# Kernel optimization log

Measured on AMD Instinct MI355X. Metric: run time of the kernel, lower is better.

## Reference

```python
import jax, jax.numpy as jnp
import numpy as np

N_NODES = 50000
N_EDGES = 800000
HID = 128


def setup_inputs() -> dict:
    key = jax.random.key(0)
    ks = jax.random.split(key, 10)
    s_msg = 1.0 / np.sqrt(2 * HID + 1)
    s_u1 = 1.0 / np.sqrt(2 * HID)
    s_u2 = 1.0 / np.sqrt(HID)
    return {
        "z": jax.random.normal(ks[0], (N_NODES, HID), dtype=jnp.float32),
        "edge_weight": jax.random.uniform(ks[1], (N_EDGES,), dtype=jnp.float32),
        "edge_src": jax.random.randint(ks[2], (N_EDGES,), 0, N_NODES),
        "edge_dst": jax.random.randint(ks[3], (N_EDGES,), 0, N_NODES),
        "Wm": jax.random.normal(ks[4], (2 * HID + 1, HID), dtype=jnp.float32) * s_msg,
        "bm": jax.random.normal(ks[5], (HID,), dtype=jnp.float32) * s_msg,
        "W1": jax.random.normal(ks[6], (2 * HID, HID), dtype=jnp.float32) * s_u1,
        "b1": jax.random.normal(ks[7], (HID,), dtype=jnp.float32) * s_u1,
        "W2": jax.random.normal(ks[8], (HID, HID), dtype=jnp.float32) * s_u2,
        "b2": jax.random.normal(ks[9], (HID,), dtype=jnp.float32) * s_u2,
    }


def reference(z, edge_weight, edge_src, edge_dst, Wm, bm, W1, b1, W2, b2):
    n, H = z.shape
    # message Linear on concat([z[u], z[v], w]) split to avoid materializing [E, 2H+1]
    Wd, Ws, ww = Wm[:H], Wm[H:2 * H], Wm[2 * H]  # [H,H], [H,H], [H]
    msgs = (z[edge_dst] @ Wd + z[edge_src] @ Ws
            + edge_weight[:, None] * ww[None, :] + bm)  # [E, H]
    # max-aggregate messages per destination node; zeros for isolated nodes
    agg = jax.ops.segment_max(msgs, edge_dst, num_segments=n)  # [n, H], -inf if empty
    deg = jax.ops.segment_sum(jnp.ones_like(edge_weight), edge_dst, num_segments=n)
    agg = jnp.where(deg[:, None] > 0, agg, jnp.zeros((), dtype=z.dtype))
    # update MLP on concat([z, agg]) split into two GEMMs
    W1a, W1b = W1[:H], W1[H:]
    hidden = jax.nn.relu(z @ W1a + agg @ W1b + b1)  # [n, H]
    return hidden @ W2 + b2  # [n, H]
```

## Files before the change

### kernel.cpp

```cpp
#include <hip/hip_runtime.h>
#include <hip/hip_bf16.h>

#define HID 128

typedef short bf16x8 __attribute__((ext_vector_type(8)));
typedef float f32x4  __attribute__((ext_vector_type(4)));
typedef unsigned short u16;
typedef unsigned long long u64;

__device__ __forceinline__ u16 f2bf(float f) {
    __hip_bfloat16 h = __float2bfloat16(f);
    return *reinterpret_cast<u16*>(&h);
}
__device__ __forceinline__ float bf2f(u16 x) {
    unsigned u = ((unsigned)x) << 16;
    return __uint_as_float(u);
}
__device__ __forceinline__ u64 pack_rec(int dst, int src, float w) {
    int wq = (int)fmaf(w, 32768.f, 0.5f);
    wq = wq > 32767 ? 32767 : wq;
    return ((u64)(unsigned)dst << 31) | ((unsigned)src << 15) | (unsigned)wq;
}


__global__ __launch_bounds__(256)
void hist_kernel(const int* __restrict__ edst, int* __restrict__ bhist,
                 int E, int nbk)
{
    __shared__ int lh[256];
    const int b = blockIdx.x;
    const int t = threadIdx.x;
    lh[t] = 0;
    __syncthreads();
    const int e0 = b * 4096;
    const int eend = min(e0 + 4096, E);
    for (int e = e0 + t; e < eend; e += 256)
        atomicAdd(&lh[edst[e] >> 8], 1);
    __syncthreads();
    if (t < nbk && lh[t] > 0) atomicAdd(&bhist[t], lh[t]);
}

__global__ __launch_bounds__(256)
void cast_scatter(const float* __restrict__ z, const float* __restrict__ Wm,
                  const float* __restrict__ W1, const float* __restrict__ W2,
                  const int* __restrict__ esrc, const int* __restrict__ edst,
                  const float* __restrict__ ew,
                  const int* __restrict__ bhist, int* __restrict__ brun,
                  u16* __restrict__ Ab, u16* __restrict__ Wt, u64* __restrict__ tmp,
                  int N, int Mp, int E, int bz, int bw, int nbk)
{
    const int b = blockIdx.x;
    const int t = threadIdx.x;
    if (b < bz) {
        const int idx8 = (b * 256 + t) * 8;
        const int row = idx8 >> 7, col = idx8 & 127;
        bf16x8 u;
        if (row < N) {
            const float4 v0 = *(const float4*)&z[(size_t)row * 128 + col];
            const float4 v1 = *(const float4*)&z[(size_t)row * 128 + col + 4];
            u[0] = (short)f2bf(v0.x); u[1] = (short)f2bf(v0.y);
            u[2] = (short)f2bf(v0.z); u[3] = (short)f2bf(v0.w);
            u[4] = (short)f2bf(v1.x); u[5] = (short)f2bf(v1.y);
            u[6] = (short)f2bf(v1.z); u[7] = (short)f2bf(v1.w);
        } else { u = bf16x8{0,0,0,0,0,0,0,0}; }
        *(bf16x8*)&Ab[(size_t)row * 256 + col] = u;
    } else if (b < bz + bw) {
        const int idx = (b - bz) * 256 + t;
        float v;
        if (idx < 32768) {
            const int nn = idx >> 7, k = idx & 127;
            v = (nn < 128) ? Wm[k * 128 + nn] : Wm[(128 + k) * 128 + (nn - 128)];
        } else if (idx < 65536) {
            const int j = idx - 32768, n = j >> 8, k = j & 255;
            v = W1[k * 128 + n];
        } else {
            const int j = idx - 65536, n = j >> 7, k = j & 127;
            v = W2[k * 128 + n];
        }
        Wt[idx] = f2bf(v);
    } else {
        __shared__ int cnt[256];
        __shared__ int rbase[256];
        __shared__ int bbase[256];
        __shared__ int ps[256];
        const int e0 = (b - bz - bw) * 4096;
        const int eend = min(e0 + 4096, E);

        const int h = (t < nbk) ? bhist[t] : 0;
        ps[t] = h;
        __syncthreads();
        for (int off = 1; off < 256; off <<= 1) {
            int add = (t >= off) ? ps[t - off] : 0;
            __syncthreads();
            ps[t] += add;
            __syncthreads();
        }
        bbase[t] = ps[t] - h;
        cnt[t] = 0;
        __syncthreads();

        if (eend - e0 == 4096) {
            int myb[16]; u64 myrec[16];
#pragma unroll
            for (int i = 0; i < 16; i++) {
                const int e = e0 + t + i * 256;
                const int d = edst[e];
                myb[i] = d >> 8;
                myrec[i] = pack_rec(d, esrc[e], ew[e]);
                atomicAdd(&cnt[myb[i]], 1);
            }
            __syncthreads();
            if (t < nbk && cnt[t] > 0) rbase[t] = bbase[t] + atomicAdd(&brun[t], cnt[t]);
            __syncthreads();
            cnt[t] = 0;
            __syncthreads();
#pragma unroll
            for (int i = 0; i < 16; i++) {
                const int r = atomicAdd(&cnt[myb[i]], 1);
                tmp[(size_t)rbase[myb[i]] + r] = myrec[i];
            }
        } else {
            for (int e = e0 + t; e < eend; e += 256)
                atomicAdd(&cnt[edst[e] >> 8], 1);
            __syncthreads();
            if (t < nbk && cnt[t] > 0) rbase[t] = bbase[t] + atomicAdd(&brun[t], cnt[t]);
            __syncthreads();
            cnt[t] = 0;
            __syncthreads();
            for (int e = e0 + t; e < eend; e += 256) {
                const int d = edst[e];
                const int bk = d >> 8;
                const int r = atomicAdd(&cnt[bk], 1);
                tmp[(size_t)rbase[bk] + r] = pack_rec(d, esrc[e], ew[e]);
            }
        }
    }
}

__global__ __launch_bounds__(256)
void sort_gemmP(const u64* __restrict__ tmp, const int* __restrict__ bhist,
                int* __restrict__ offsets, unsigned* __restrict__ s_ew,
                int N, int E, int nbk,
                const u16* __restrict__ Ab, const u16* __restrict__ Wds_t,
                u16* __restrict__ Pb, int Mp)
{
    const int t = threadIdx.x;

    if (blockIdx.x < (unsigned)nbk) {
        __shared__ int cnt[256];
        __shared__ int cur[256];
        __shared__ int ps[256];
        const int b = blockIdx.x;
        const int n0 = b << 8;
        const int nhi = min(256, N - n0);

        const int h = (t < nbk) ? bhist[t] : 0;
        ps[t] = h;
        __syncthreads();
        for (int off = 1; off < 256; off <<= 1) {
            int add = (t >= off) ? ps[t - off] : 0;
            __syncthreads();
            ps[t] += add;
            __syncthreads();
        }
        const int base = (b > 0) ? ps[b - 1] : 0;
        const int endp = ps[b];
        cnt[t] = 0;
        __syncthreads();

        for (int r = base + t; r < endp; r += 256)
            atomicAdd(&cnt[(int)(tmp[r] >> 31) - n0], 1);
        __syncthreads();

        const int v = cnt[t];
        ps[t] = v;
        __syncthreads();
        for (int off = 1; off < 256; off <<= 1) {
            int add = (t >= off) ? ps[t - off] : 0;
            __syncthreads();
            ps[t] += add;
            __syncthreads();
        }
        cur[t] = base + ps[t] - v;
        __syncthreads();

        if (t < nhi) offsets[n0 + t] = cur[t];
        if (t == 0 && n0 + nhi == N) offsets[N] = E;

        for (int r = base + t; r < endp; r += 256) {
            const u64 rec = tmp[r];
            const int local = (int)(rec >> 31) - n0;
            const int pos = atomicAdd(&cur[local], 1);
            s_ew[pos] = (unsigned)(rec & 0x7FFFFFFFu);
        }
    } else {
        __shared__ u16 As[64 * 136];
        const int row0 = (blockIdx.x - nbk) * 64;
        const int wv = t >> 6, lane = t & 63;
        const int wy = wv & 1, wx = wv >> 1;
        const int q = lane >> 4, n = lane & 15;

#pragma unroll
        for (int i = 0; i < 4; i++) {
            const int chunk = i * 256 + t;
            const int row = chunk >> 4;
            const int c8 = chunk & 15;
            *(bf16x8*)&As[row * 136 + c8 * 8] =
                *(const bf16x8*)&Ab[(size_t)(row0 + row) * 256 + c8 * 8];
        }
        __syncthreads();

        const u16* pAl = As + (wy * 32 + n) * 136 + q * 8;
        const u16* pB = Wds_t + (size_t)(wx * 128 + n) * 128 + q * 8;

        f32x4 acc[2][8];
#pragma unroll
        for (int i = 0; i < 2; i++)
#pragma unroll
            for (int j = 0; j < 8; j++) acc[i][j] = f32x4{0.f, 0.f, 0.f, 0.f};

#pragma unroll
        for (int kk = 0; kk < 128; kk += 32) {
            bf16x8 a0 = *(const bf16x8*)(pAl + kk);
            bf16x8 a1 = *(const bf16x8*)(pAl + 16 * 136 + kk);
            bf16x8 bfr[8];
#pragma unroll
            for (int ni = 0; ni < 8; ni++)
                bfr[ni] = *(const bf16x8*)(pB + (size_t)ni * 16 * 128 + kk);
#pragma unroll
            for (int ni = 0; ni < 8; ni++) {
                acc[0][ni] = __builtin_amdgcn_mfma_f32_16x16x32_bf16(a0, bfr[ni], acc[0][ni], 0, 0, 0);
                acc[1][ni] = __builtin_amdgcn_mfma_f32_16x16x32_bf16(a1, bfr[ni], acc[1][ni], 0, 0, 0);
            }
        }

#pragma unroll
        for (int mi = 0; mi < 2; mi++) {
#pragma unroll
            for (int ni = 0; ni < 8; ni++) {
                const int rbase2 = row0 + wy * 32 + mi * 16 + q * 4;
                const int c = wx * 128 + ni * 16 + n;
#pragma unroll
                for (int r = 0; r < 4; r++)
                    Pb[(size_t)(rbase2 + r) * 256 + c] = f2bf(acc[mi][ni][r]);
            }
        }
    }
}

__global__ __launch_bounds__(256)
void aggregate_kernel(const u16* __restrict__ Pb,
                      const float* __restrict__ bm,
                      const float* __restrict__ ww,
                      const int* __restrict__ offsets,
                      const unsigned* __restrict__ s_ew,
                      u16* __restrict__ Ab, int N, int Mp)
{
    const int t = threadIdx.x;
    const int lane = t & 63;
    const int c0 = (lane & 15) * 8;
    const int nd = blockIdx.x * 16 + ((t >> 6) << 2) + (lane >> 4);
    if (nd >= Mp) return;

    u16* dst = &Ab[(size_t)nd * 256 + 128 + c0];

    int start = 0, end = 0;
    if (nd < N) { start = offsets[nd]; end = offsets[nd + 1]; }

    if (end <= start) {
        bf16x8 zv = {0, 0, 0, 0, 0, 0, 0, 0};
        *(bf16x8*)dst = zv;
        return;
    }

    float wwv[8];
    {
        const float4 wa = *(const float4*)&ww[c0];
        const float4 wb = *(const float4*)&ww[c0 + 4];
        wwv[0] = wa.x; wwv[1] = wa.y; wwv[2] = wa.z; wwv[3] = wa.w;
        wwv[4] = wb.x; wwv[5] = wb.y; wwv[6] = wb.z; wwv[7] = wb.w;
    }

    const float kq = 1.f / 32768.f;
    float m[8];
#pragma unroll
    for (int j = 0; j < 8; j++) m[j] = -INFINITY;

    const int last = end - 1;
    for (int eb = start; eb < end; eb += 8) {
        unsigned u[8];
#pragma unroll
        for (int i = 0; i < 8; i++) {
            int e = eb + i; if (e > last) e = last;
            u[i] = s_ew[e];
        }
        bf16x8 p[8];
#pragma unroll
        for (int i = 0; i < 8; i++)
            p[i] = *(const bf16x8*)&Pb[(size_t)(u[i] >> 15) * 256 + 128 + c0];
#pragma unroll
        for (int i = 0; i < 8; i++) {
            const float w = (float)(u[i] & 32767u) * kq;
#pragma unroll
            for (int j = 0; j < 8; j++)
                m[j] = fmaxf(m[j], fmaf(w, wwv[j], bf2f((u16)p[i][j])));
        }
    }

    const bf16x8 zd = *(const bf16x8*)&Pb[(size_t)nd * 256 + c0];
    float bmv[8];
    {
        const float4 ba = *(const float4*)&bm[c0];
        const float4 bb = *(const float4*)&bm[c0 + 4];
        bmv[0] = ba.x; bmv[1] = ba.y; bmv[2] = ba.z; bmv[3] = ba.w;
        bmv[4] = bb.x; bmv[5] = bb.y; bmv[6] = bb.z; bmv[7] = bb.w;
    }
    bf16x8 outv;
#pragma unroll
    for (int j = 0; j < 8; j++)
        outv[j] = (short)f2bf(bf2f((u16)zd[j]) + bmv[j] + m[j]);
    *(bf16x8*)dst = outv;
}

__global__ __launch_bounds__(256)
void gemm_HO(const u16* __restrict__ Ab, const u16* __restrict__ W1t,
             const float* __restrict__ b1, const u16* __restrict__ W2t,
             const float* __restrict__ b2, float* __restrict__ out, int Mstore)
{
    __shared__ u16 smem[64 * 264];

    const int row0 = blockIdx.x * 64;
    const int tid = threadIdx.x;
    const int wv = tid >> 6, lane = tid & 63;
    const int wy = wv & 1, wx = wv >> 1;
    const int q = lane >> 4, n = lane & 15;

#pragma unroll
    for (int i = 0; i < 8; i++) {
        const int chunk = i * 256 + tid;
        const int row = chunk >> 5;
        const int c8 = chunk & 31;
        *(bf16x8*)&smem[row * 264 + c8 * 8] =
            *(const bf16x8*)&Ab[(size_t)(row0 + row) * 256 + c8 * 8];
    }
    __syncthreads();

    f32x4 acc[2][4];

    {
        const u16* pAl = smem + (wy * 32 + n) * 264 + q * 8;
        const u16* pB = W1t + (size_t)(wx * 64 + n) * 256 + q * 8;

#pragma unroll
        for (int i = 0; i < 2; i++)
#pragma unroll
            for (int j = 0; j < 4; j++) acc[i][j] = f32x4{0.f, 0.f, 0.f, 0.f};

#pragma unroll
        for (int kk = 0; kk < 256; kk += 32) {
            bf16x8 b0 = *(const bf16x8*)(pB + kk);
            bf16x8 b1f = *(const bf16x8*)(pB + 16 * 256 + kk);
            bf16x8 b2f = *(const bf16x8*)(pB + 32 * 256 + kk);
            bf16x8 b3f = *(const bf16x8*)(pB + 48 * 256 + kk);
            bf16x8 a0 = *(const bf16x8*)(pAl + kk);
            bf16x8 a1 = *(const bf16x8*)(pAl + 16 * 264 + kk);
            acc[0][0] = __builtin_amdgcn_mfma_f32_16x16x32_bf16(a0, b0,  acc[0][0], 0, 0, 0);
            acc[0][1] = __builtin_amdgcn_mfma_f32_16x16x32_bf16(a0, b1f, acc[0][1], 0, 0, 0);
            acc[0][2] = __builtin_amdgcn_mfma_f32_16x16x32_bf16(a0, b2f, acc[0][2], 0, 0, 0);
            acc[0][3] = __builtin_amdgcn_mfma_f32_16x16x32_bf16(a0, b3f, acc[0][3], 0, 0, 0);
            acc[1][0] = __builtin_amdgcn_mfma_f32_16x16x32_bf16(a1, b0,  acc[1][0], 0, 0, 0);
            acc[1][1] = __builtin_amdgcn_mfma_f32_16x16x32_bf16(a1, b1f, acc[1][1], 0, 0, 0);
            acc[1][2] = __builtin_amdgcn_mfma_f32_16x16x32_bf16(a1, b2f, acc[1][2], 0, 0, 0);
            acc[1][3] = __builtin_amdgcn_mfma_f32_16x16x32_bf16(a1, b3f, acc[1][3], 0, 0, 0);
        }
    }
    __syncthreads();

#pragma unroll
    for (int mi = 0; mi < 2; mi++) {
#pragma unroll
        for (int ni = 0; ni < 4; ni++) {
            const int rl = wy * 32 + mi * 16 + q * 4;
            const int c = wx * 64 + ni * 16 + n;
#pragma unroll
            for (int r = 0; r < 4; r++) {
                float v = acc[mi][ni][r] + b1[c];
                smem[(rl + r) * 136 + c] = f2bf(fmaxf(v, 0.f));
            }
        }
    }
    __syncthreads();

    {
        const u16* pB = W2t + (size_t)(wx * 64 + n) * 128 + q * 8;
        const u16* pHl = smem + (wy * 32 + n) * 136 + q * 8;

#pragma unroll
        for (int i = 0; i < 2; i++)
#pragma unroll
            for (int j = 0; j < 4; j++) acc[i][j] = f32x4{0.f, 0.f, 0.f, 0.f};

#pragma unroll
        for (int kk = 0; kk < 128; kk += 32) {
            bf16x8 b0 = *(const bf16x8*)(pB + kk);
            bf16x8 b1f = *(const bf16x8*)(pB + 16 * 128 + kk);
            bf16x8 b2f = *(const bf16x8*)(pB + 32 * 128 + kk);
            bf16x8 b3f = *(const bf16x8*)(pB + 48 * 128 + kk);
            bf16x8 a0 = *(const bf16x8*)(pHl + kk);
            bf16x8 a1 = *(const bf16x8*)(pHl + 16 * 136 + kk);
            acc[0][0] = __builtin_amdgcn_mfma_f32_16x16x32_bf16(a0, b0,  acc[0][0], 0, 0, 0);
            acc[0][1] = __builtin_amdgcn_mfma_f32_16x16x32_bf16(a0, b1f, acc[0][1], 0, 0, 0);
            acc[0][2] = __builtin_amdgcn_mfma_f32_16x16x32_bf16(a0, b2f, acc[0][2], 0, 0, 0);
            acc[0][3] = __builtin_amdgcn_mfma_f32_16x16x32_bf16(a0, b3f, acc[0][3], 0, 0, 0);
            acc[1][0] = __builtin_amdgcn_mfma_f32_16x16x32_bf16(a1, b0,  acc[1][0], 0, 0, 0);
            acc[1][1] = __builtin_amdgcn_mfma_f32_16x16x32_bf16(a1, b1f, acc[1][1], 0, 0, 0);
            acc[1][2] = __builtin_amdgcn_mfma_f32_16x16x32_bf16(a1, b2f, acc[1][2], 0, 0, 0);
            acc[1][3] = __builtin_amdgcn_mfma_f32_16x16x32_bf16(a1, b3f, acc[1][3], 0, 0, 0);
        }

#pragma unroll
        for (int mi = 0; mi < 2; mi++) {
#pragma unroll
            for (int ni = 0; ni < 4; ni++) {
                const int rbase = row0 + wy * 32 + mi * 16 + q * 4;
                const int c = wx * 64 + ni * 16 + n;
#pragma unroll
                for (int r = 0; r < 4; r++) {
                    const int rr = rbase + r;
                    if (rr >= Mstore) continue;
                    out[(size_t)rr * 128 + c] = acc[mi][ni][r] + b2[c];
                }
            }
        }
    }
}

extern "C" void kernel_launch(void* const* d_in, const int* in_sizes, int n_in,
                              void* d_out, int out_size, void* d_ws, size_t ws_size,
                              hipStream_t stream) {
    const float* z    = (const float*)d_in[0];
    const float* ew   = (const float*)d_in[1];
    const int*   esrc = (const int*)d_in[2];
    const int*   edst = (const int*)d_in[3];
    const float* Wm   = (const float*)d_in[4];
    const float* bm   = (const float*)d_in[5];
    const float* W1   = (const float*)d_in[6];
    const float* b1   = (const float*)d_in[7];
    const float* W2   = (const float*)d_in[8];
    const float* b2   = (const float*)d_in[9];
    float* out = (float*)d_out;

    const int N  = in_sizes[0] / HID;
    const int E  = in_sizes[1];
    const int Mp = ((N + 63) / 64) * 64;
    const int nbk = (N + 255) / 256;

    char* w = (char*)d_ws;
    u16*  Ab      = (u16*)w;      w += (size_t)Mp * 256 * 2;
    u16*  Pb      = (u16*)w;      w += (size_t)Mp * 256 * 2;
    u16*  Wt      = (u16*)w;      w += (size_t)81920 * 2;
    int*  offsets = (int*)w;      w += (size_t)(N + 64) * 4;
    int*  bhist   = (int*)w;      w += 256 * 4;
    int*  brun    = (int*)w;      w += 256 * 4;
    unsigned* s_ew = (unsigned*)w; w += (size_t)E * 4;
    u64*  tmp     = (u64*)w;      w += (size_t)E * 8;

    const int bz8 = (Mp * 16 + 255) / 256;
    const int bw  = (81920 + 255) / 256;
    const int nsc = (E + 4095) / 4096;

    hipMemsetAsync(bhist, 0, 512 * sizeof(int), stream);
    hist_kernel<<<nsc, 256, 0, stream>>>(edst, bhist, E, nbk);
    cast_scatter<<<bz8 + bw + nsc, 256, 0, stream>>>(z, Wm, W1, W2, esrc, edst, ew,
                                                     bhist, brun, Ab, Wt, tmp,
                                                     N, Mp, E, bz8, bw, nbk);
    sort_gemmP<<<nbk + Mp / 64, 256, 0, stream>>>(tmp, bhist, offsets, s_ew,
                                                  N, E, nbk, Ab, Wt, Pb, Mp);
    aggregate_kernel<<<(Mp + 15) / 16, 256, 0, stream>>>(Pb, bm, Wm + 256 * 128,
                                                         offsets, s_ew, Ab, N, Mp);
    gemm_HO<<<Mp / 64, 256, 0, stream>>>(Ab, Wt + 32768, b1, Wt + 65536, b2, out, N);
}
```

Baseline: 209.1 us.

## Fold destination-side message GEMM and bias into update weights W1

The destination projection z[dst]@Wd is constant within each max-aggregation segment, so it is pulled out of the max and folded into the update MLP. A fused weight W1a + Wd·W1b and a bias b1 + bm·W1b are precomputed in an extra block, which halves the per-node P GEMM and the Pb buffer to 128 columns. Isolated nodes get an explicit -(z@Wd + bm) correction computed with a scalar loop so the zero-aggregation semantics still hold. The exchange is extra bf16 rounding through the fused weights and a slow path for zero-degree nodes.

```diff
diff --git a/kernel.cpp b/kernel.cpp
--- a/kernel.cpp
+++ b/kernel.cpp
@@ -141,8 +141,11 @@
 void sort_gemmP(const u64* __restrict__ tmp, const int* __restrict__ bhist,
                 int* __restrict__ offsets, unsigned* __restrict__ s_ew,
                 int N, int E, int nbk,
-                const u16* __restrict__ Ab, const u16* __restrict__ Wds_t,
-                u16* __restrict__ Pb, int Mp)
+                const u16* __restrict__ Ab, const u16* __restrict__ Wt,
+                u16* __restrict__ Pb, int Mp, int nP,
+                const float* __restrict__ Wm, const float* __restrict__ b1,
+                const float* __restrict__ bm,
+                u16* __restrict__ W1f, float* __restrict__ bprime)
 {
     const int t = threadIdx.x;
 
@@ -193,7 +196,7 @@
             const int pos = atomicAdd(&cur[local], 1);
             s_ew[pos] = (unsigned)(rec & 0x7FFFFFFFu);
         }
-    } else {
+    } else if (blockIdx.x < (unsigned)(nbk + nP)) {
         __shared__ u16 As[64 * 136];
         const int row0 = (blockIdx.x - nbk) * 64;
         const int wv = t >> 6, lane = t & 63;
@@ -211,22 +214,79 @@
         __syncthreads();
 
         const u16* pAl = As + (wy * 32 + n) * 136 + q * 8;
-        const u16* pB = Wds_t + (size_t)(wx * 128 + n) * 128 + q * 8;
-
-        f32x4 acc[2][8];
+        const u16* pB = Wt + (size_t)(128 + wx * 64 + n) * 128 + q * 8;
+
+        f32x4 acc[2][4];
 #pragma unroll
         for (int i = 0; i < 2; i++)
 #pragma unroll
-            for (int j = 0; j < 8; j++) acc[i][j] = f32x4{0.f, 0.f, 0.f, 0.f};
+            for (int j = 0; j < 4; j++) acc[i][j] = f32x4{0.f, 0.f, 0.f, 0.f};
 
 #pragma unroll
         for (int kk = 0; kk < 128; kk += 32) {
             bf16x8 a0 = *(const bf16x8*)(pAl + kk);
             bf16x8 a1 = *(const bf16x8*)(pAl + 16 * 136 + kk);
+            bf16x8 bfr[4];
+#pragma unroll
+            for (int ni = 0; ni < 4; ni++)
+                bfr[ni] = *(const bf16x8*)(pB + (size_t)ni * 16 * 128 + kk);
+#pragma unroll
+            for (int ni = 0; ni < 4; ni++) {
+                acc[0][ni] = __builtin_amdgcn_mfma_f32_16x16x32_bf16(a0, bfr[ni], acc[0][ni], 0, 0, 0);
+                acc[1][ni] = __builtin_amdgcn_mfma_f32_16x16x32_bf16(a1, bfr[ni], acc[1][ni], 0, 0, 0);
+            }
+        }
+
+#pragma unroll
+        for (int mi = 0; mi < 2; mi++) {
+#pragma unroll
+            for (int ni = 0; ni < 4; ni++) {
+                const int rbase2 = row0 + wy * 32 + mi * 16 + q * 4;
+                const int c = wx * 64 + ni * 16 + n;
+#pragma unroll
+                for (int r = 0; r < 4; r++)
+                    Pb[(size_t)(rbase2 + r) * 128 + c] = f2bf(acc[mi][ni][r]);
+            }
+        }
+    } else {
+        const u16* W1t = Wt + 32768;
+        const int wv = t >> 6, lane = t & 63;
+        const int q = lane >> 4, n16 = lane & 15;
+
+#pragma unroll
+        for (int i = 0; i < 8; i++) {
+            const int idx8 = (i * 256 + t) * 8;
+            const int row = idx8 >> 7, c = idx8 & 127;
+            *(bf16x8*)&W1f[row * 256 + 128 + c] =
+                *(const bf16x8*)&W1t[row * 256 + 128 + c];
+        }
+
+        const int r0 = wv * 32;
+        const u16* pA = W1t + (size_t)(r0 + n16) * 256 + 128 + q * 8;
+
+        f32x4 acc[2][8];
+#pragma unroll
+        for (int i = 0; i < 2; i++)
+#pragma unroll
+            for (int j = 0; j < 8; j++) acc[i][j] = f32x4{0.f, 0.f, 0.f, 0.f};
+
+#pragma unroll
+        for (int kk = 0; kk < 128; kk += 32) {
+            bf16x8 a0 = *(const bf16x8*)(pA + kk);
+            bf16x8 a1 = *(const bf16x8*)(pA + 16 * 256 + kk);
             bf16x8 bfr[8];
 #pragma unroll
-            for (int ni = 0; ni < 8; ni++)
-                bfr[ni] = *(const bf16x8*)(pB + (size_t)ni * 16 * 128 + kk);
+            for (int ni = 0; ni < 8; ni++) {
+                const float* src = &Wm[(size_t)(ni * 16 + n16) * 128 + kk + q * 8];
+                const float4 v0 = *(const float4*)src;
+                const float4 v1 = *(const float4*)(src + 4);
+                bf16x8 bb;
+                bb[0] = (short)f2bf(v0.x); bb[1] = (short)f2bf(v0.y);
+                bb[2] = (short)f2bf(v0.z); bb[3] = (short)f2bf(v0.w);
+                bb[4] = (short)f2bf(v1.x); bb[5] = (short)f2bf(v1.y);
+                bb[6] = (short)f2bf(v1.z); bb[7] = (short)f2bf(v1.w);
+                bfr[ni] = bb;
+            }
 #pragma unroll
             for (int ni = 0; ni < 8; ni++) {
                 acc[0][ni] = __builtin_amdgcn_mfma_f32_16x16x32_bf16(a0, bfr[ni], acc[0][ni], 0, 0, 0);
@@ -238,12 +298,22 @@
         for (int mi = 0; mi < 2; mi++) {
 #pragma unroll
             for (int ni = 0; ni < 8; ni++) {
-                const int rbase2 = row0 + wy * 32 + mi * 16 + q * 4;
-                const int c = wx * 128 + ni * 16 + n;
-#pragma unroll
-                for (int r = 0; r < 4; r++)
-                    Pb[(size_t)(rbase2 + r) * 256 + c] = f2bf(acc[mi][ni][r]);
-            }
+                const int row = r0 + mi * 16 + q * 4;
+                const int c = ni * 16 + n16;
+#pragma unroll
+                for (int r = 0; r < 4; r++) {
+                    const int rr = row + r;
+                    W1f[rr * 256 + c] =
+                        f2bf(acc[mi][ni][r] + bf2f(W1t[rr * 256 + c]));
+                }
+            }
+        }
+
+        if (t < 128) {
+            float s = b1[t];
+            for (int c = 0; c < 128; c++)
+                s = fmaf(bm[c], bf2f(W1t[t * 256 + 128 + c]), s);
+            bprime[t] = s;
         }
     }
 }
@@ -254,7 +324,9 @@
                       const float* __restrict__ ww,
                       const int* __restrict__ offsets,
                       const unsigned* __restrict__ s_ew,
-                      u16* __restrict__ Ab, int N, int Mp)
+                      u16* __restrict__ Ab,
+                      const u16* __restrict__ WdT,
+                      int N, int Mp)
 {
     const int t = threadIdx.x;
     const int lane = t & 63;
@@ -264,12 +336,30 @@
 
     u16* dst = &Ab[(size_t)nd * 256 + 128 + c0];
 
-    int start = 0, end = 0;
-    if (nd < N) { start = offsets[nd]; end = offsets[nd + 1]; }
-
-    if (end <= start) {
+    if (nd >= N) {
         bf16x8 zv = {0, 0, 0, 0, 0, 0, 0, 0};
         *(bf16x8*)dst = zv;
+        return;
+    }
+
+    const int start = offsets[nd];
+    const int end   = offsets[nd + 1];
+
+    if (end <= start) {
+        float acc8[8];
+#pragma unroll
+        for (int j = 0; j < 8; j++) acc8[j] = 0.f;
+        for (int k = 0; k < 128; k++) {
+            const float zk = bf2f(Ab[(size_t)nd * 256 + k]);
+#pragma unroll
+            for (int j = 0; j < 8; j++)
+                acc8[j] = fmaf(zk, bf2f(WdT[(size_t)(c0 + j) * 128 + k]), acc8[j]);
+        }
+        bf16x8 outv;
+#pragma unroll
+        for (int j = 0; j < 8; j++)
+            outv[j] = (short)f2bf(-(acc8[j] + bm[c0 + j]));
+        *(bf16x8*)dst = outv;
         return;
     }
 
@@ -297,7 +387,7 @@
         bf16x8 p[8];
 #pragma unroll
         for (int i = 0; i < 8; i++)
-            p[i] = *(const bf16x8*)&Pb[(size_t)(u[i] >> 15) * 256 + 128 + c0];
+            p[i] = *(const bf16x8*)&Pb[(size_t)(u[i] >> 15) * 128 + c0];
 #pragma unroll
         for (int i = 0; i < 8; i++) {
             const float w = (float)(u[i] & 32767u) * kq;
@@ -307,18 +397,10 @@
         }
     }
 
-    const bf16x8 zd = *(const bf16x8*)&Pb[(size_t)nd * 256 + c0];
-    float bmv[8];
-    {
-        const float4 ba = *(const float4*)&bm[c0];
-        const float4 bb = *(const float4*)&bm[c0 + 4];
-        bmv[0] = ba.x; bmv[1] = ba.y; bmv[2] = ba.z; bmv[3] = ba.w;
-        bmv[4] = bb.x; bmv[5] = bb.y; bmv[6] = bb.z; bmv[7] = bb.w;
-    }
     bf16x8 outv;
 #pragma unroll
     for (int j = 0; j < 8; j++)
-        outv[j] = (short)f2bf(bf2f((u16)zd[j]) + bmv[j] + m[j]);
+        outv[j] = (short)f2bf(m[j]);
     *(bf16x8*)dst = outv;
 }
 
@@ -454,11 +536,14 @@
     const int E  = in_sizes[1];
     const int Mp = ((N + 63) / 64) * 64;
     const int nbk = (N + 255) / 256;
+    const int nP  = Mp / 64;
 
     char* w = (char*)d_ws;
     u16*  Ab      = (u16*)w;      w += (size_t)Mp * 256 * 2;
-    u16*  Pb      = (u16*)w;      w += (size_t)Mp * 256 * 2;
+    u16*  Pb      = (u16*)w;      w += (size_t)Mp * 128 * 2;
     u16*  Wt      = (u16*)w;      w += (size_t)81920 * 2;
+    u16*  W1f     = (u16*)w;      w += (size_t)32768 * 2;
+    float* bprime = (float*)w;    w += 128 * 4;
     int*  offsets = (int*)w;      w += (size_t)(N + 64) * 4;
     int*  bhist   = (int*)w;      w += 256 * 4;
     int*  brun    = (int*)w;      w += 256 * 4;
@@ -474,9 +559,11 @@
     cast_scatter<<<bz8 + bw + nsc, 256, 0, stream>>>(z, Wm, W1, W2, esrc, edst, ew,
                                                      bhist, brun, Ab, Wt, tmp,
                                                      N, Mp, E, bz8, bw, nbk);
-    sort_gemmP<<<nbk + Mp / 64, 256, 0, stream>>>(tmp, bhist, offsets, s_ew,
-                                                  N, E, nbk, Ab, Wt, Pb, Mp);
+    sort_gemmP<<<nbk + nP + 1, 256, 0, stream>>>(tmp, bhist, offsets, s_ew,
+                                                 N, E, nbk, Ab, Wt, Pb, Mp, nP,
+                                                 Wm, b1, bm, W1f, bprime);
     aggregate_kernel<<<(Mp + 15) / 16, 256, 0, stream>>>(Pb, bm, Wm + 256 * 128,
-                                                         offsets, s_ew, Ab, N, Mp);
-    gemm_HO<<<Mp / 64, 256, 0, stream>>>(Ab, Wt + 32768, b1, Wt + 65536, b2, out, N);
-}
+                                                         offsets, s_ew, Ab, Wt,
+                                                         N, Mp);
+    gemm_HO<<<Mp / 64, 256, 0, stream>>>(Ab, W1f, bprime, Wt + 65536, b2, out, N);
+}
```

Result: faster. 204.8 us (-2.1%).
